# Optimization experiments

Hardware: AMD Instinct MI355X
Metric: run time of the kernel (lower is better)

The kernel has to match this reference:

```python
import jax, jax.numpy as jnp
import numpy as np

VOCAB, EMBED, HIDDEN, NUM_CLASSES, PAD_IDX = 50257, 128, 128, 4, 0
B, T = 256, 512


def setup_inputs() -> dict:
    key = jax.random.key(0)
    ks = jax.random.split(key, 10)
    x = jax.random.randint(ks[0], (B, T), 0, VOCAB)
    h0 = jnp.zeros((B, HIDDEN), dtype=jnp.float32)
    # embedding: uniform(-0.1, 0.1), pad row zeroed (matches init_weights)
    emb = jax.random.uniform(ks[1], (VOCAB, EMBED), jnp.float32, -0.1, 0.1)
    emb = emb.at[PAD_IDX].set(0.0)
    def xavier(k, shape):
        fan_out, fan_in = shape
        bound = float(np.sqrt(6.0 / (fan_in + fan_out)))
        return jax.random.uniform(k, shape, jnp.float32, -bound, bound)
    W_ih = xavier(ks[2], (HIDDEN, EMBED))      # rnn.weight_ih_l0
    W_hh = xavier(ks[3], (HIDDEN, HIDDEN))     # rnn.weight_hh_l0
    b_ih = jnp.zeros((HIDDEN,), jnp.float32)
    b_hh = jnp.zeros((HIDDEN,), jnp.float32)
    W1 = xavier(ks[4], (2 * HIDDEN, HIDDEN))   # output_layer1
    b1 = jnp.zeros((2 * HIDDEN,), jnp.float32)
    W2 = xavier(ks[5], (NUM_CLASSES, 2 * HIDDEN))  # output_layer2
    b2 = jnp.zeros((NUM_CLASSES,), jnp.float32)
    return {"x": x, "h0": h0, "emb": emb, "W_ih": W_ih, "W_hh": W_hh,
            "b_ih": b_ih, "b_hh": b_hh, "W1": W1, "b1": b1, "W2": W2, "b2": b2}


def reference(x, h0, emb, W_ih, W_hh, b_ih, b_hh, W1, b1, W2, b2):
    # Embedding lookup (dropout layers are identity in eval mode)
    embedded = emb[x]                                    # [B, T, E]
    # Precompute input projection for every step, then scan the recurrence.
    x_proj = jnp.einsum('bte,he->bth', embedded, W_ih) + b_ih + b_hh  # [B, T, H]
    x_proj_t = jnp.swapaxes(x_proj, 0, 1)                # [T, B, H]

    def step(h, xp):
        h_new = jnp.tanh(xp + h @ W_hh.T)                # [B, H]
        return h_new, None

    last_hidden, _ = jax.lax.scan(step, h0, x_proj_t)    # [B, H]
    # MLP head: Linear -> ReLU -> Linear
    hidden_mlp = jax.nn.relu(last_hidden @ W1.T + b1)    # [B, 2H]
    logits = hidden_mlp @ W2.T + b2                      # [B, C]
    return (logits, last_hidden)
```

## Files before the change

kernel.cpp:

```cpp
#include <hip/hip_runtime.h>
#include <hip/hip_bf16.h>
#include <math.h>

#define BB 256
#define TT 512
#define EE 128
#define HH 128
#define NC 4
#define MM (BB * TT)

typedef __bf16 bf16x8 __attribute__((ext_vector_type(8)));
typedef __bf16 bf16x4 __attribute__((ext_vector_type(4)));
typedef float  f32x4  __attribute__((ext_vector_type(4)));
typedef float  f32x2  __attribute__((ext_vector_type(2)));

__device__ __forceinline__ float fast_tanh(float x) {
    float t = __builtin_amdgcn_exp2f(x * 2.885390081777927f);
    return 1.f - 2.f * __builtin_amdgcn_rcpf(1.f + t);
}

__device__ __forceinline__ void bar_lds() {
    asm volatile("s_waitcnt lgkmcnt(0)\n\ts_barrier" ::: "memory");
}

template <typename XPT>
__global__ __launch_bounds__(256, 2) void embed_gemm(
    const int* __restrict__ x, const float* __restrict__ emb,
    const float* __restrict__ Wih, const float* __restrict__ bih,
    const float* __restrict__ bhh, XPT* __restrict__ xpout)
{
    const int tid = threadIdx.x;
    const int m0  = blockIdx.x * 64;

    const int LDA = 72;
    __shared__ __bf16 Ah[64 * 72];
    __shared__ __bf16 Al[64 * 72];
    __shared__ __bf16 Wh[128 * 72];
    __shared__ __bf16 Wl[128 * 72];
    __shared__ float  bias_s[128];
    __shared__ int    gix[64];

    if (tid < 64)  gix[tid] = x[m0 + tid];
    if (tid < 128) bias_s[tid] = bih[tid] + bhh[tid];

    const int lane = tid & 63, wid = tid >> 6;
    const int col  = lane & 15, quad = lane >> 4;

    f32x4 acc[8];
#pragma unroll
    for (int nt = 0; nt < 8; ++nt) acc[nt] = f32x4{0.f, 0.f, 0.f, 0.f};

    __syncthreads();

#pragma unroll
    for (int half = 0; half < 2; ++half) {
#pragma unroll
        for (int it = 0; it < 8; ++it) {
            int c   = it * 256 + tid;
            int row = c >> 4;
            int seg = c & 15;
            float4 wv = ((const float4*)Wih)[row * 32 + half * 16 + seg];
            bf16x4 wh, wl;
            wh[0] = (__bf16)wv.x; wl[0] = (__bf16)(wv.x - (float)wh[0]);
            wh[1] = (__bf16)wv.y; wl[1] = (__bf16)(wv.y - (float)wh[1]);
            wh[2] = (__bf16)wv.z; wl[2] = (__bf16)(wv.z - (float)wh[2]);
            wh[3] = (__bf16)wv.w; wl[3] = (__bf16)(wv.w - (float)wh[3]);
            *(bf16x4*)&Wh[row * LDA + seg * 4] = wh;
            *(bf16x4*)&Wl[row * LDA + seg * 4] = wl;
        }
#pragma unroll
        for (int it = 0; it < 4; ++it) {
            int c   = it * 256 + tid;
            int row = c >> 4;
            int seg = c & 15;
            int gi  = gix[row];
            float4 av = ((const float4*)emb)[(size_t)gi * 32 + half * 16 + seg];
            bf16x4 ah, al;
            ah[0] = (__bf16)av.x; al[0] = (__bf16)(av.x - (float)ah[0]);
            ah[1] = (__bf16)av.y; al[1] = (__bf16)(av.y - (float)ah[1]);
            ah[2] = (__bf16)av.z; al[2] = (__bf16)(av.z - (float)ah[2]);
            ah[3] = (__bf16)av.w; al[3] = (__bf16)(av.w - (float)ah[3]);
            *(bf16x4*)&Ah[row * LDA + seg * 4] = ah;
            *(bf16x4*)&Al[row * LDA + seg * 4] = al;
        }
        __syncthreads();

#pragma unroll
        for (int kk = 0; kk < 2; ++kk) {
            int ra = (wid * 16 + col) * LDA + kk * 32 + quad * 8;
            bf16x8 afh = *(const bf16x8*)&Ah[ra];
            bf16x8 afl = *(const bf16x8*)&Al[ra];
#pragma unroll
            for (int nt = 0; nt < 8; ++nt) {
                int ro = (nt * 16 + col) * LDA + kk * 32 + quad * 8;
                bf16x8 wfh = *(const bf16x8*)&Wh[ro];
                bf16x8 wfl = *(const bf16x8*)&Wl[ro];
                acc[nt] = __builtin_amdgcn_mfma_f32_16x16x32_bf16(afh, wfh, acc[nt], 0, 0, 0);
                acc[nt] = __builtin_amdgcn_mfma_f32_16x16x32_bf16(afl, wfh, acc[nt], 0, 0, 0);
                acc[nt] = __builtin_amdgcn_mfma_f32_16x16x32_bf16(afh, wfl, acc[nt], 0, 0, 0);
            }
        }
        if (half == 0) __syncthreads();
    }

#pragma unroll
    for (int nt = 0; nt < 8; ++nt) {
        int m = m0 + wid * 16 + quad * 4;
        int n = nt * 16 + col;
        float bs = bias_s[n];
#pragma unroll
        for (int r = 0; r < 4; ++r)
            xpout[(size_t)(m + r) * 128 + n] = (XPT)(acc[nt][r] + bs);
    }
}

template <typename XPT>
__global__ __launch_bounds__(256, 1) void rnn_scan(
    const XPT* __restrict__ xp, const float* __restrict__ Whh,
    const float* __restrict__ h0, float* __restrict__ hlast)
{
    const int b    = blockIdx.x;
    const int tid  = threadIdx.x;
    const int q    = tid >> 6;
    const int lane = tid & 63;

    __shared__ float h_s[128];
    __shared__ float part[4 * 128];

    f32x4 wA[8], wB[8];
    {
        const float* r0 = Whh + (size_t)lane * 128 + q * 32;
        const float* r1 = Whh + (size_t)(lane + 64) * 128 + q * 32;
#pragma unroll
        for (int c = 0; c < 8; ++c) {
            wA[c] = *(const f32x4*)(r0 + c * 4);
            wB[c] = *(const f32x4*)(r1 + c * 4);
        }
    }

    if (tid < 128) h_s[tid] = h0[b * 128 + tid];

    const XPT* xpb = xp + (size_t)b * (TT * 128);
    float xv[8];
#pragma unroll
    for (int s = 0; s < 8; ++s)
        xv[s] = (tid < 128) ? (float)xpb[s * 128 + tid] : 0.f;
    bar_lds();

    for (int tw = 0; tw < TT; tw += 8) {
        asm volatile("" : "+v"(wA[0]), "+v"(wA[1]), "+v"(wA[2]), "+v"(wA[3]),
                          "+v"(wA[4]), "+v"(wA[5]), "+v"(wA[6]), "+v"(wA[7]),
                          "+v"(wB[0]), "+v"(wB[1]), "+v"(wB[2]), "+v"(wB[3]),
                          "+v"(wB[4]), "+v"(wB[5]), "+v"(wB[6]), "+v"(wB[7]));
#pragma unroll
        for (int ts = 0; ts < 8; ++ts) {
            const float* hq = &h_s[q * 32];
            f32x4 h4[8];
#pragma unroll
            for (int u = 0; u < 8; ++u) h4[u] = *(const f32x4*)&hq[u * 4];

            f32x4 aA = f32x4{0.f, 0.f, 0.f, 0.f};
            f32x4 aB = f32x4{0.f, 0.f, 0.f, 0.f};
#pragma unroll
            for (int u = 0; u < 8; ++u) {
                aA += wA[u] * h4[u];
                aB += wB[u] * h4[u];
            }
            part[q * 128 + lane]      = (aA[0] + aA[1]) + (aA[2] + aA[3]);
            part[q * 128 + 64 + lane] = (aB[0] + aB[1]) + (aB[2] + aB[3]);
            bar_lds();
            if (tid < 128) {
                float s = (part[tid] + part[128 + tid])
                        + (part[256 + tid] + part[384 + tid]);
                h_s[tid] = fast_tanh(s + xv[ts]);
                if (tw + 8 < TT)
                    xv[ts] = (float)xpb[(size_t)(tw + 8 + ts) * 128 + tid];
            }
            bar_lds();
        }
    }
    if (tid < 128) hlast[b * 128 + tid] = h_s[tid];
}

__global__ __launch_bounds__(256, 2) void mlp_head(
    const float* __restrict__ hlast, const float* __restrict__ W1,
    const float* __restrict__ b1, const float* __restrict__ W2,
    const float* __restrict__ b2, float* __restrict__ out)
{
    const int b = blockIdx.x, tid = threadIdx.x;
    __shared__ float h_row[128];
    __shared__ float hid[256];

    if (tid < 128) {
        float hv = hlast[b * 128 + tid];
        h_row[tid] = hv;
        out[1024 + b * 128 + tid] = hv;
    }
    __syncthreads();

    {
        float acc = b1[tid];
        const float4* wrow = (const float4*)(W1 + (size_t)tid * 128);
#pragma unroll
        for (int k4 = 0; k4 < 32; ++k4) {
            float4 wv = wrow[k4];
            acc += wv.x * h_row[k4 * 4 + 0] + wv.y * h_row[k4 * 4 + 1]
                 + wv.z * h_row[k4 * 4 + 2] + wv.w * h_row[k4 * 4 + 3];
        }
        hid[tid] = fmaxf(acc, 0.f);
    }
    __syncthreads();

    const int wv = tid >> 6, lane = tid & 63;
    float s = 0.f;
#pragma unroll
    for (int qq = 0; qq < 4; ++qq)
        s += hid[qq * 64 + lane] * W2[wv * 256 + qq * 64 + lane];
#pragma unroll
    for (int off = 32; off > 0; off >>= 1) s += __shfl_down(s, off);
    if (lane == 0) out[b * 4 + wv] = s + b2[wv];
}

extern "C" void kernel_launch(void* const* d_in, const int* in_sizes, int n_in,
                              void* d_out, int out_size, void* d_ws, size_t ws_size,
                              hipStream_t stream)
{
    const int*   x   = (const int*)d_in[0];
    const float* h0  = (const float*)d_in[1];
    const float* emb = (const float*)d_in[2];
    const float* Wih = (const float*)d_in[3];
    const float* Whh = (const float*)d_in[4];
    const float* bih = (const float*)d_in[5];
    const float* bhh = (const float*)d_in[6];
    const float* W1  = (const float*)d_in[7];
    const float* b1  = (const float*)d_in[8];
    const float* W2  = (const float*)d_in[9];
    const float* b2  = (const float*)d_in[10];
    float* out = (float*)d_out;

    const size_t xp_f32_bytes = (size_t)MM * 128 * sizeof(float);
    const size_t hl_bytes     = (size_t)BB * 128 * sizeof(float);

    if (ws_size >= xp_f32_bytes + hl_bytes) {
        float* xpw = (float*)d_ws;
        float* hl  = (float*)((char*)d_ws + xp_f32_bytes);
        embed_gemm<float><<<MM / 64, 256, 0, stream>>>(x, emb, Wih, bih, bhh, xpw);
        rnn_scan<float><<<BB, 256, 0, stream>>>(xpw, Whh, h0, hl);
        mlp_head<<<BB, 256, 0, stream>>>(hl, W1, b1, W2, b2, out);
    } else {
        __bf16* xpw = (__bf16*)d_ws;
        float*  hl  = (float*)((char*)d_ws + (size_t)MM * 128 * sizeof(__bf16));
        embed_gemm<__bf16><<<MM / 64, 256, 0, stream>>>(x, emb, Wih, bih, bhh, xpw);
        rnn_scan<__bf16><<<BB, 256, 0, stream>>>(xpw, Whh, h0, hl);
        mlp_head<<<BB, 256, 0, stream>>>(hl, W1, b1, W2, b2, out);
    }
}
```

Measured before the change: 283.9 us.

## Load embedding rows directly into registers and stage GEMM output through LDS

The embed GEMM no longer stages the gathered embedding rows in LDS. Each lane reads its A fragment straight from global memory and splits it into bf16 hi/lo in registers, which cuts shared memory enough to allow three blocks per CU. The epilogue writes accumulators to an LDS buffer that reuses the weight space, then emits coalesced 16-byte row stores to xp. The scan kernel swaps the custom waitcnt+barrier for __syncthreads and moves the register-pinning asm out of the loop, which could change the scheduling of the latency-critical recurrence.

```diff
diff --git a/kernel.cpp b/kernel.cpp
--- a/kernel.cpp
+++ b/kernel.cpp
@@ -12,19 +12,14 @@
 typedef __bf16 bf16x8 __attribute__((ext_vector_type(8)));
 typedef __bf16 bf16x4 __attribute__((ext_vector_type(4)));
 typedef float  f32x4  __attribute__((ext_vector_type(4)));
-typedef float  f32x2  __attribute__((ext_vector_type(2)));
 
 __device__ __forceinline__ float fast_tanh(float x) {
     float t = __builtin_amdgcn_exp2f(x * 2.885390081777927f);
     return 1.f - 2.f * __builtin_amdgcn_rcpf(1.f + t);
 }
 
-__device__ __forceinline__ void bar_lds() {
-    asm volatile("s_waitcnt lgkmcnt(0)\n\ts_barrier" ::: "memory");
-}
-
 template <typename XPT>
-__global__ __launch_bounds__(256, 2) void embed_gemm(
+__global__ __launch_bounds__(256, 3) void embed_gemm(
     const int* __restrict__ x, const float* __restrict__ emb,
     const float* __restrict__ Wih, const float* __restrict__ bih,
     const float* __restrict__ bhh, XPT* __restrict__ xpout)
@@ -32,25 +27,25 @@
     const int tid = threadIdx.x;
     const int m0  = blockIdx.x * 64;
 
-    const int LDA = 72;
-    __shared__ __bf16 Ah[64 * 72];
-    __shared__ __bf16 Al[64 * 72];
-    __shared__ __bf16 Wh[128 * 72];
-    __shared__ __bf16 Wl[128 * 72];
-    __shared__ float  bias_s[128];
-    __shared__ int    gix[64];
-
-    if (tid < 64)  gix[tid] = x[m0 + tid];
+    const int LDW = 72;
+    const int LDE = 132;
+    __shared__ __align__(16) char smem[36864 + 512];
+    __bf16* Wh     = (__bf16*)smem;
+    __bf16* Wl     = (__bf16*)(smem + 18432);
+    float*  epi    = (float*)smem;
+    float*  bias_s = (float*)(smem + 36864);
+
     if (tid < 128) bias_s[tid] = bih[tid] + bhh[tid];
 
     const int lane = tid & 63, wid = tid >> 6;
     const int col  = lane & 15, quad = lane >> 4;
 
+    const int gi = x[m0 + wid * 16 + col];
+    const float* arow = emb + (size_t)gi * 128;
+
     f32x4 acc[8];
 #pragma unroll
     for (int nt = 0; nt < 8; ++nt) acc[nt] = f32x4{0.f, 0.f, 0.f, 0.f};
-
-    __syncthreads();
 
 #pragma unroll
     for (int half = 0; half < 2; ++half) {
@@ -65,34 +60,25 @@
             wh[1] = (__bf16)wv.y; wl[1] = (__bf16)(wv.y - (float)wh[1]);
             wh[2] = (__bf16)wv.z; wl[2] = (__bf16)(wv.z - (float)wh[2]);
             wh[3] = (__bf16)wv.w; wl[3] = (__bf16)(wv.w - (float)wh[3]);
-            *(bf16x4*)&Wh[row * LDA + seg * 4] = wh;
-            *(bf16x4*)&Wl[row * LDA + seg * 4] = wl;
-        }
-#pragma unroll
-        for (int it = 0; it < 4; ++it) {
-            int c   = it * 256 + tid;
-            int row = c >> 4;
-            int seg = c & 15;
-            int gi  = gix[row];
-            float4 av = ((const float4*)emb)[(size_t)gi * 32 + half * 16 + seg];
-            bf16x4 ah, al;
-            ah[0] = (__bf16)av.x; al[0] = (__bf16)(av.x - (float)ah[0]);
-            ah[1] = (__bf16)av.y; al[1] = (__bf16)(av.y - (float)ah[1]);
-            ah[2] = (__bf16)av.z; al[2] = (__bf16)(av.z - (float)ah[2]);
-            ah[3] = (__bf16)av.w; al[3] = (__bf16)(av.w - (float)ah[3]);
-            *(bf16x4*)&Ah[row * LDA + seg * 4] = ah;
-            *(bf16x4*)&Al[row * LDA + seg * 4] = al;
+            *(bf16x4*)&Wh[row * LDW + seg * 4] = wh;
+            *(bf16x4*)&Wl[row * LDW + seg * 4] = wl;
         }
         __syncthreads();
 
 #pragma unroll
         for (int kk = 0; kk < 2; ++kk) {
-            int ra = (wid * 16 + col) * LDA + kk * 32 + quad * 8;
-            bf16x8 afh = *(const bf16x8*)&Ah[ra];
-            bf16x8 afl = *(const bf16x8*)&Al[ra];
+            const float* ap = arow + half * 64 + kk * 32 + quad * 8;
+            f32x4 a0 = *(const f32x4*)ap;
+            f32x4 a1 = *(const f32x4*)(ap + 4);
+            bf16x8 afh, afl;
+#pragma unroll
+            for (int u = 0; u < 4; ++u) {
+                afh[u]     = (__bf16)a0[u]; afl[u]     = (__bf16)(a0[u] - (float)afh[u]);
+                afh[u + 4] = (__bf16)a1[u]; afl[u + 4] = (__bf16)(a1[u] - (float)afh[u + 4]);
+            }
 #pragma unroll
             for (int nt = 0; nt < 8; ++nt) {
-                int ro = (nt * 16 + col) * LDA + kk * 32 + quad * 8;
+                int ro = (nt * 16 + col) * LDW + kk * 32 + quad * 8;
                 bf16x8 wfh = *(const bf16x8*)&Wh[ro];
                 bf16x8 wfl = *(const bf16x8*)&Wl[ro];
                 acc[nt] = __builtin_amdgcn_mfma_f32_16x16x32_bf16(afh, wfh, acc[nt], 0, 0, 0);
@@ -100,17 +86,33 @@
                 acc[nt] = __builtin_amdgcn_mfma_f32_16x16x32_bf16(afh, wfl, acc[nt], 0, 0, 0);
             }
         }
-        if (half == 0) __syncthreads();
+        __syncthreads();
     }
 
 #pragma unroll
     for (int nt = 0; nt < 8; ++nt) {
-        int m = m0 + wid * 16 + quad * 4;
         int n = nt * 16 + col;
         float bs = bias_s[n];
 #pragma unroll
         for (int r = 0; r < 4; ++r)
-            xpout[(size_t)(m + r) * 128 + n] = (XPT)(acc[nt][r] + bs);
+            epi[(wid * 16 + quad * 4 + r) * LDE + n] = acc[nt][r] + bs;
+    }
+    __syncthreads();
+
+#pragma unroll
+    for (int it = 0; it < 8; ++it) {
+        int c   = it * 256 + tid;
+        int row = c >> 5;
+        int cf  = c & 31;
+        f32x4 v = *(const f32x4*)&epi[row * LDE + cf * 4];
+        if (sizeof(XPT) == 4) {
+            *(f32x4*)&((float*)xpout)[(size_t)(m0 + row) * 128 + cf * 4] = v;
+        } else {
+            bf16x4 bv;
+            bv[0] = (__bf16)v[0]; bv[1] = (__bf16)v[1];
+            bv[2] = (__bf16)v[2]; bv[3] = (__bf16)v[3];
+            *(bf16x4*)&((__bf16*)xpout)[(size_t)(m0 + row) * 128 + cf * 4] = bv;
+        }
     }
 }
 
@@ -137,6 +139,9 @@
             wB[c] = *(const f32x4*)(r1 + c * 4);
         }
     }
+#pragma unroll
+    for (int c = 0; c < 8; ++c)
+        asm volatile("" : "+v"(wA[c]), "+v"(wB[c]));
 
     if (tid < 128) h_s[tid] = h0[b * 128 + tid];
 
@@ -145,13 +150,9 @@
 #pragma unroll
     for (int s = 0; s < 8; ++s)
         xv[s] = (tid < 128) ? (float)xpb[s * 128 + tid] : 0.f;
-    bar_lds();
+    __syncthreads();
 
     for (int tw = 0; tw < TT; tw += 8) {
-        asm volatile("" : "+v"(wA[0]), "+v"(wA[1]), "+v"(wA[2]), "+v"(wA[3]),
-                          "+v"(wA[4]), "+v"(wA[5]), "+v"(wA[6]), "+v"(wA[7]),
-                          "+v"(wB[0]), "+v"(wB[1]), "+v"(wB[2]), "+v"(wB[3]),
-                          "+v"(wB[4]), "+v"(wB[5]), "+v"(wB[6]), "+v"(wB[7]));
 #pragma unroll
         for (int ts = 0; ts < 8; ++ts) {
             const float* hq = &h_s[q * 32];
@@ -168,7 +169,7 @@
             }
             part[q * 128 + lane]      = (aA[0] + aA[1]) + (aA[2] + aA[3]);
             part[q * 128 + 64 + lane] = (aB[0] + aB[1]) + (aB[2] + aB[3]);
-            bar_lds();
+            __syncthreads();
             if (tid < 128) {
                 float s = (part[tid] + part[128 + tid])
                         + (part[256 + tid] + part[384 + tid]);
@@ -176,7 +177,7 @@
                 if (tw + 8 < TT)
                     xv[ts] = (float)xpb[(size_t)(tw + 8 + ts) * 128 + tid];
             }
-            bar_lds();
+            __syncthreads();
         }
     }
     if (tid < 128) hlast[b * 128 + tid] = h_s[tid];
```

Result: faster. 276.8 us (-2.5%).
